# Optimization experiments

Hardware: AMD Instinct MI355X
Metric: run time of the kernel (lower is better)

The kernel has to match this reference:

```python
import jax, jax.numpy as jnp
import numpy as np

B, V, C, H, W, D = 1, 3, 32, 320, 320, 32


def setup_inputs() -> dict:
    key = jax.random.key(0)
    ks = jax.random.split(key, 14)
    feats = jax.random.normal(ks[0], (B, V, C, H, W), jnp.float32)
    # Valid pinhole projections: P = [[K @ [R|t]], [0,0,0,1]], identity rotation,
    # horizontal baselines sized so the warp stays mostly in-image over the depth range.
    K = np.array([[400.0, 0.0, W / 2.0], [0.0, 400.0, H / 2.0], [0.0, 0.0, 1.0]])
    mats = []
    for tx in (0.0, 100.0, -100.0):
        Rt = np.eye(4)
        Rt[0, 3] = tx
        P = np.eye(4)
        P[:3, :4] = K @ Rt[:3, :4]
        mats.append(P)
    proj = jnp.asarray(np.broadcast_to(np.stack(mats)[None], (B, V, 4, 4)).copy(), jnp.float32)
    planes = jnp.linspace(425.0, 935.0, D, dtype=jnp.float32)
    depth_values = jnp.broadcast_to(planes[None, :, None, None], (B, D, H, W)).astype(jnp.float32)
    s = 0.05  # small init so exp(reg_cost) stays well-scaled
    W0 = s * jax.random.normal(ks[1], (8, C, 3, 3), jnp.float32)
    Ws1 = s * jax.random.normal(ks[2], (8, 8, 3, 3), jnp.float32)
    W1 = s * jax.random.normal(ks[3], (16, 8, 3, 3), jnp.float32)
    Ws2 = s * jax.random.normal(ks[4], (16, 16, 3, 3), jnp.float32)
    W2 = s * jax.random.normal(ks[5], (32, 16, 3, 3), jnp.float32)
    Ws3 = s * jax.random.normal(ks[6], (32, 32, 3, 3), jnp.float32)
    W3 = s * jax.random.normal(ks[7], (64, 32, 3, 3), jnp.float32)
    Ws4 = s * jax.random.normal(ks[8], (64, 64, 3, 3), jnp.float32)
    U4 = s * jax.random.normal(ks[9], (32, 64, 1, 1), jnp.float32)
    U3 = s * jax.random.normal(ks[10], (16, 32, 1, 1), jnp.float32)
    U2 = s * jax.random.normal(ks[11], (8, 16, 1, 1), jnp.float32)
    Wout = s * jax.random.normal(ks[12], (1, 8, 3, 3), jnp.float32)
    return dict(feats=feats, proj=proj, depth_values=depth_values, W0=W0, Ws1=Ws1,
                W1=W1, Ws2=Ws2, W2=W2, Ws3=Ws3, W3=W3, Ws4=Ws4, U4=U4, U3=U3, U2=U2, Wout=Wout)


def _conv(x, w, stride=1):
    return jax.lax.conv_general_dilated(x, w, (stride, stride), 'SAME',
                                        dimension_numbers=('NCHW', 'OIHW', 'NCHW'))


def _up2(x):
    return jnp.repeat(jnp.repeat(x, 2, axis=2), 2, axis=3)


def _bilinear(img, x, y):
    # img [C,H,W]; x,y [N] pixel coords; zero padding, align_corners semantics
    Cc, Hh, Ww = img.shape
    x0 = jnp.floor(x)
    y0 = jnp.floor(y)
    wx = x - x0
    wy = y - y0

    def tap(xi, yi):
        valid = ((xi >= 0) & (xi <= Ww - 1) & (yi >= 0) & (yi <= Hh - 1)).astype(img.dtype)
        xc = jnp.clip(xi, 0, Ww - 1).astype(jnp.int32)
        yc = jnp.clip(yi, 0, Hh - 1).astype(jnp.int32)
        return img[:, yc, xc] * valid  # [C,N]

    return (tap(x0, y0) * (1 - wx) * (1 - wy) + tap(x0 + 1, y0) * wx * (1 - wy)
            + tap(x0, y0 + 1) * (1 - wx) * wy + tap(x0 + 1, y0 + 1) * wx * wy)


def _forward(feats, proj, depth_values, W0, Ws1, W1, Ws2, W2, Ws3, W3, Ws4, U4, U3, U2, Wout):
    Bn, Vn, Cn, Hn, Wn = feats.shape
    Dn = depth_values.shape[1]
    N = Hn * Wn
    relu = jax.nn.relu
    ref = feats[:, 0]
    ref_sq = ref * ref
    # Precompute per-src-view rotated pixel rays and translations.
    inv_ref = jnp.linalg.inv(proj[:, 0])                       # [B,4,4]
    rel = jnp.einsum('bvij,bjk->bvik', proj[:, 1:], inv_ref)   # [B,V-1,4,4]
    rot, trans = rel[:, :, :3, :3], rel[:, :, :3, 3]
    ys, xs = jnp.meshgrid(jnp.arange(Hn), jnp.arange(Wn), indexing='ij')
    pix = jnp.stack([xs.ravel(), ys.ravel(), jnp.ones(N)], 0).astype(feats.dtype)  # [3,N]
    rot_pix = jnp.einsum('bvij,jn->bvin', rot, pix)            # [B,V-1,3,N]

    def regularize(x, s1, s2, s3, s4):
        c1 = relu(_conv(x, W0) + _conv(s1, Ws1))
        c2 = relu(_conv(c1, W1, 2) + _conv(s2, Ws2))
        c3 = relu(_conv(c2, W2, 2) + _conv(s3, Ws3))
        c4 = relu(_conv(c3, W3, 2) + _conv(s4, Ws4))
        u3 = c3 + _up2(_conv(c4, U4))
        u2 = c2 + _up2(_conv(u3, U3))
        u1 = c1 + _up2(_conv(u2, U2))
        return _conv(u1, Wout), c1, c2, c3, c4

    def step(carry, depth_slice):  # depth_slice [B,H,W]
        s1, s2, s3, s4, exp_sum, depth_img, max_prob = carry
        vol_sum, vol_sq = ref, ref_sq
        dflat = depth_slice.reshape(Bn, 1, N)
        for v in range(Vn - 1):
            xyz = rot_pix[:, v] * dflat + trans[:, v, :, None]   # [B,3,N]
            px = xyz[:, 0] / xyz[:, 2]
            py = xyz[:, 1] / xyz[:, 2]
            warped = jax.vmap(_bilinear)(feats[:, v + 1], px, py).reshape(Bn, Cn, Hn, Wn)
            vol_sum = vol_sum + warped
            vol_sq = vol_sq + warped * warped
        variance = vol_sq / Vn - (vol_sum / Vn) ** 2
        cost, s1, s2, s3, s4 = regularize(variance, s1, s2, s3, s4)
        prob = jnp.exp(cost)                                     # [B,1,H,W]
        max_prob = jnp.maximum(max_prob, prob)                   # == flag*prob + (1-flag)*max
        depth_img = depth_img + depth_slice[:, None] * prob
        exp_sum = exp_sum + prob
        return (s1, s2, s3, s4, exp_sum, depth_img, max_prob), None

    z = lambda c, h, w: jnp.zeros((Bn, c, h, w), feats.dtype)
    init = (z(8, Hn, Wn), z(16, Hn // 2, Wn // 2), z(32, Hn // 4, Wn // 4), z(64, Hn // 8, Wn // 8),
            z(1, Hn, Wn), z(1, Hn, Wn), z(1, Hn, Wn))
    carry, _ = jax.lax.scan(step, init, jnp.moveaxis(depth_values, 1, 0))
    _, _, _, _, exp_sum, depth_img, max_prob = carry
    es = exp_sum + 1e-10
    depth_map = (depth_img / es)[:, 0]
    prob_map = (max_prob / es)[:, 0]
    return jnp.stack([depth_map, prob_map], axis=1)  # [B,2,H,W]


def reference(feats, proj, depth_values, W0, Ws1, W1, Ws2, W2, Ws3, W3, Ws4, U4, U3, U2, Wout):
    return _forward(feats, proj, depth_values, W0, Ws1, W1, Ws2, W2, Ws3, W3, Ws4, U4, U3, U2, Wout)
```

## Files before the change

kernel.cpp:

```cpp
#include <hip/hip_runtime.h>
#include <hip/hip_fp16.h>
#include <math.h>

#define HH 320
#define WW 320
#define NP (HH*WW)
#define CC 32
#define DD 32

#define H2 160
#define W2 160
#define N2 (H2*W2)
#define H4 80
#define W4 80
#define N4 (H4*W4)
#define H8 40
#define W8 40
#define N8 (H8*W8)

#define HALO 18
#define NHALO (HALO*HALO)

#define C1SZ (8*NP)
#define C2SZ (16*N2)
#define C3SZ (32*N4)
#define C4SZ (64*N8)

#define SMEM_FLOATS 5344

#define OFF_REL   0
#define OFF_C1R   64
#define OFF_C2R   (OFF_C1R + 5*C1SZ)
#define OFF_C3R   (OFF_C2R + 4*C2SZ)
#define OFF_C4R   (OFF_C3R + 3*C3SZ)
#define OFF_ESUM  (OFF_C4R + 2*C4SZ)
#define OFF_DIMG  (OFF_ESUM + NP)
#define OFF_MAXP  (OFF_DIMG + NP)
#define OFF_ACCE  (OFF_MAXP + NP)
#define OFF_FT    OFF_ACCE
#define OFF_END   (OFF_FT + (3*CC*NP)/2)

__global__ void k_prep(const float* __restrict__ proj, float* __restrict__ rel) {
    if (threadIdx.x != 0 || blockIdx.x != 0) return;
    float a[4][4], inv[4][4];
#pragma unroll
    for (int i = 0; i < 4; i++)
#pragma unroll
        for (int j = 0; j < 4; j++) {
            a[i][j] = proj[i*4 + j];
            inv[i][j] = (i == j) ? 1.0f : 0.0f;
        }
#pragma unroll
    for (int c = 0; c < 4; c++) {
        float s = 1.0f / a[c][c];
#pragma unroll
        for (int j = 0; j < 4; j++) { a[c][j] *= s; inv[c][j] *= s; }
#pragma unroll
        for (int r = 0; r < 4; r++) if (r != c) {
            float f = a[r][c];
#pragma unroll
            for (int j = 0; j < 4; j++) {
                a[r][j] -= f * a[c][j];
                inv[r][j] -= f * inv[c][j];
            }
        }
    }
#pragma unroll
    for (int v = 1; v < 3; v++) {
        const float* P = proj + v*16;
        float rm[3][4];
#pragma unroll
        for (int i = 0; i < 3; i++)
#pragma unroll
            for (int j = 0; j < 4; j++) {
                float s = 0.0f;
#pragma unroll
                for (int k = 0; k < 4; k++) s += P[i*4 + k] * inv[k][j];
                rm[i][j] = s;
            }
        float* o = rel + (v-1)*12;
        o[0]=rm[0][0]; o[1]=rm[0][1]; o[2]=rm[0][2];
        o[3]=rm[1][0]; o[4]=rm[1][1]; o[5]=rm[1][2];
        o[6]=rm[2][0]; o[7]=rm[2][1]; o[8]=rm[2][2];
        o[9]=rm[0][3]; o[10]=rm[1][3]; o[11]=rm[2][3];
    }
}

__global__ __launch_bounds__(256) void k_transpose(const float* __restrict__ feats,
                                                   __half* __restrict__ featsT) {
    __shared__ float lds[32][65];
    int g = blockIdx.x;
    int v = g / 1600;
    int p0 = (g - v*1600) * 64;
    const float* src = feats + (size_t)v*CC*NP + p0;
    for (int i = threadIdx.x; i < 32*64; i += 256) {
        int c = i >> 6, pp = i & 63;
        lds[c][pp] = src[(size_t)c*NP + pp];
    }
    __syncthreads();
    __half* dst = featsT + ((size_t)v*NP + p0)*32;
    int pp = threadIdx.x >> 2, cq = (threadIdx.x & 3) * 8;
    __half2 h[4];
#pragma unroll
    for (int j = 0; j < 4; j++)
        h[j] = __floats2half2_rn(lds[cq+2*j][pp], lds[cq+2*j+1][pp]);
    *(float4*)(dst + (size_t)pp*32 + cq) = *(float4*)h;
}

__device__ __forceinline__ void set_hline8(const __half* base, float* s) {
    float4 raw = *(const float4*)base;
    const __half2* h2 = (const __half2*)&raw;
#pragma unroll
    for (int j = 0; j < 4; j++) {
        float2 f = __half22float2(h2[j]);
        s[2*j]     = f.x;
        s[2*j + 1] = f.y;
    }
}
__device__ __forceinline__ void acc_hline8(const __half* base, float w, float* t) {
    float4 raw = *(const float4*)base;
    const __half2* h2 = (const __half2*)&raw;
#pragma unroll
    for (int j = 0; j < 4; j++) {
        float2 f = __half22float2(h2[j]);
        t[2*j]     += f.x * w;
        t[2*j + 1] += f.y * w;
    }
}

__device__ __forceinline__ int band_tile(int blk) { return (blk & 7) * 50 + (blk >> 3); }


__device__ void stageA(int blk, int d, int useT,
        const float* __restrict__ feats, const __half* __restrict__ featsT,
        const float* __restrict__ rel,
        const float* __restrict__ depthv, const float* __restrict__ c1r,
        const float* __restrict__ W0, const float* __restrict__ Ws1,
        float* smem) {
    __half2* pbuf = (__half2*)smem;
    float* fbuf = smem;
    const float* dslice = depthv + (size_t)d * NP;
    const float* s1 = c1r + (size_t)((d+4)%5) * C1SZ;
    float* c1out = (float*)c1r + (size_t)(d%5) * C1SZ;

    int L = band_tile(blk);
    int bx = L % 20, by = L / 20;
    int ox0 = bx*16, oy0 = by*16;

    const float inv3 = 1.0f / 3.0f;

    int opx = threadIdx.x & 15, opy = threadIdx.x >> 4;
    int obase = opy*HALO + opx;
    int outp = (oy0 + opy)*WW + ox0 + opx;

#pragma unroll 1
    for (int s = 0; s < 2; s++) {
        int hp = threadIdx.x + s*256;
        if (hp >= NHALO) break;
        int hy = hp / HALO, hx = hp - hy*HALO;
        int gy = oy0 + hy - 1, gx = ox0 + hx - 1;
        if (gy < 0 || gy >= HH || gx < 0 || gx >= WW) {
            __half2 z = __floats2half2_rn(0.0f, 0.0f);
#pragma unroll 1
            for (int c = 0; c < 16; c++) pbuf[c*NHALO + hp] = z;
            continue;
        }
        int p = gy*WW + gx;
        float depth = dslice[p];
        float fx = (float)gx, fy = (float)gy;

#pragma unroll 1
        for (int q = 0; q < 4; q++) {
            int cb = q * 8;
            float sum[8], sq[8];
            if (useT) {
                set_hline8(featsT + ((size_t)p << 5) + cb, sum);
#pragma unroll
                for (int c = 0; c < 8; c++) sq[c] = sum[c]*sum[c];
#pragma unroll
                for (int v = 0; v < 2; v++) {
                    const float* r = rel + v*12;
                    float X = (r[0]*fx + r[1]*fy + r[2]) * depth + r[9];
                    float Y = (r[3]*fx + r[4]*fy + r[5]) * depth + r[10];
                    float Z = (r[6]*fx + r[7]*fy + r[8]) * depth + r[11];
                    float iz = 1.0f / Z;
                    float px = X * iz, py = Y * iz;
                    float x0f = floorf(px), y0f = floorf(py);
                    float wx = px - x0f, wy = py - y0f;
                    int x0 = (int)x0f, y0 = (int)y0f;
                    const __half* fv = featsT + (size_t)(v+1)*CC*NP;
                    float t[8];
#pragma unroll
                    for (int c = 0; c < 8; c++) t[c] = 0.0f;
#pragma unroll
                    for (int tp = 0; tp < 4; tp++) {
                        int xi = x0 + (tp & 1), yi = y0 + (tp >> 1);
                        float wgt = ((tp & 1) ? wx : 1.0f - wx)
                                  * ((tp >> 1) ? wy : 1.0f - wy);
                        bool valid = (xi >= 0) && (xi <= WW-1) &&
                                     (yi >= 0) && (yi <= HH-1);
                        int xc = min(max(xi, 0), WW-1);
                        int yc = min(max(yi, 0), HH-1);
                        acc_hline8(fv + ((size_t)(yc*WW + xc) << 5) + cb,
                                   valid ? wgt : 0.0f, t);
                    }
#pragma unroll
                    for (int c = 0; c < 8; c++) { sum[c] += t[c]; sq[c] += t[c]*t[c]; }
                }
            } else {
#pragma unroll
                for (int c = 0; c < 8; c++) {
                    float rv = feats[(cb+c)*NP + p];
                    sum[c] = rv; sq[c] = rv*rv;
                }
#pragma unroll
                for (int v = 0; v < 2; v++) {
                    const float* r = rel + v*12;
                    float X = (r[0]*fx + r[1]*fy + r[2]) * depth + r[9];
                    float Y = (r[3]*fx + r[4]*fy + r[5]) * depth + r[10];
                    float Z = (r[6]*fx + r[7]*fy + r[8]) * depth + r[11];
                    float iz = 1.0f / Z;
                    float px = X * iz, py = Y * iz;
                    float x0f = floorf(px), y0f = floorf(py);
                    float wx = px - x0f, wy = py - y0f;
                    int x0 = (int)x0f, y0 = (int)y0f;
                    bool vax = (x0 >= 0) && (x0 < WW), vbx = (x0 >= -1) && (x0 < WW-1);
                    bool vay = (y0 >= 0) && (y0 < HH), vby = (y0 >= -1) && (y0 < HH-1);
                    int xa = min(max(x0, 0), WW-1), xb = min(max(x0+1, 0), WW-1);
                    int ya = min(max(y0, 0), HH-1), yb = min(max(y0+1, 0), HH-1);
                    int o0 = ya*WW + xa, o1 = ya*WW + xb;
                    int o2 = yb*WW + xa, o3 = yb*WW + xb;
                    float w0 = (vax && vay) ? (1.0f-wx)*(1.0f-wy) : 0.0f;
                    float w1 = (vbx && vay) ? wx*(1.0f-wy) : 0.0f;
                    float w2 = (vax && vby) ? (1.0f-wx)*wy : 0.0f;
                    float w3 = (vbx && vby) ? wx*wy : 0.0f;
                    const float* fb = feats + (size_t)(v+1)*CC*NP;
#pragma unroll 1
                    for (int c = 0; c < 8; c++) {
                        const float* b = fb + (cb+c)*NP;
                        float tv = b[o0]*w0 + b[o1]*w1 + b[o2]*w2 + b[o3]*w3;
                        sum[c] += tv; sq[c] += tv*tv;
                    }
                }
            }
#pragma unroll
            for (int c = 0; c < 4; c++) {
                float m0 = sum[2*c] * inv3,   v0 = sq[2*c] * inv3 - m0*m0;
                float m1 = sum[2*c+1] * inv3, v1 = sq[2*c+1] * inv3 - m1*m1;
                pbuf[(q*4 + c)*NHALO + hp] = __floats2half2_rn(v0, v1);
            }
        }
    }
    __syncthreads();

    float acc[8];
#pragma unroll
    for (int o = 0; o < 8; o++) acc[o] = 0.0f;

#pragma unroll 1
    for (int cp = 0; cp < 16; cp++) {
        float t0[9], t1[9];
#pragma unroll
        for (int ky = 0; ky < 3; ky++)
#pragma unroll
            for (int kx = 0; kx < 3; kx++) {
                __half2 h = pbuf[cp*NHALO + obase + ky*HALO + kx];
                t0[ky*3+kx] = __low2float(h);
                t1[ky*3+kx] = __high2float(h);
            }
#pragma unroll
        for (int o = 0; o < 8; o++) {
            const float* w0 = W0 + (o*32 + 2*cp)*9;
            float a = acc[o];
#pragma unroll
            for (int k = 0; k < 9; k++) a += t0[k] * w0[k];
#pragma unroll
            for (int k = 0; k < 9; k++) a += t1[k] * w0[9 + k];
            acc[o] = a;
        }
    }
    __syncthreads();

#pragma unroll 1
    for (int hp = threadIdx.x; hp < NHALO; hp += 256) {
        int hy = hp / HALO, hx = hp - hy*HALO;
        int gy = oy0 + hy - 1, gx = ox0 + hx - 1;
        bool v = (gy >= 0) && (gy < HH) && (gx >= 0) && (gx < WW);
        int p = v ? gy*WW + gx : 0;
#pragma unroll
        for (int c = 0; c < 8; c++) fbuf[c*NHALO + hp] = v ? s1[c*NP + p] : 0.0f;
    }
    __syncthreads();
#pragma unroll 1
    for (int ci = 0; ci < 8; ci++) {
        float t[9];
#pragma unroll
        for (int ky = 0; ky < 3; ky++)
#pragma unroll
            for (int kx = 0; kx < 3; kx++) t[ky*3+kx] = fbuf[ci*NHALO + obase + ky*HALO + kx];
#pragma unroll
        for (int o = 0; o < 8; o++) {
            const float* w = Ws1 + (o*8 + ci)*9;
            float a = acc[o];
#pragma unroll
            for (int k = 0; k < 9; k++) a += t[k] * w[k];
            acc[o] = a;
        }
    }
#pragma unroll
    for (int o = 0; o < 8; o++) c1out[o*NP + outp] = fmaxf(acc[o], 0.0f);
}

__device__ void stageB(int blk, int d,
        const float* __restrict__ c1r, const float* __restrict__ c2r_,
        const float* __restrict__ W1, const float* __restrict__ Ws2) {
    const float* c1 = c1r + (size_t)(d%5) * C1SZ;
    const float* s2 = c2r_ + (size_t)((d+3)%4) * C2SZ;
    float* c2 = (float*)c2r_ + (size_t)(d%4) * C2SZ;
    int p = (blk % 100)*256 + threadIdx.x;
    int og = blk / 100;
    int y = p / W2, x = p - y*W2;
    int offsA[9]; float mskA[9];
#pragma unroll
    for (int k = 0; k < 9; k++) {
        int yy = 2*y + k/3, xx = 2*x + k%3;
        bool v = (yy < HH) && (xx < WW);
        offsA[k] = v ? yy*WW + xx : 0;
        mskA[k] = v ? 1.0f : 0.0f;
    }
    int offsB[9]; float mskB[9];
#pragma unroll
    for (int k = 0; k < 9; k++) {
        int yy = y + k/3 - 1, xx = x + k%3 - 1;
        bool v = (yy >= 0) && (yy < H2) && (xx >= 0) && (xx < W2);
        offsB[k] = v ? yy*W2 + xx : 0;
        mskB[k] = v ? 1.0f : 0.0f;
    }
    float acc[8];
#pragma unroll
    for (int o = 0; o < 8; o++) acc[o] = 0.0f;
#pragma unroll 1
    for (int ci = 0; ci < 8; ci++) {
        const float* b = c1 + ci*NP;
        float t[9];
#pragma unroll
        for (int k = 0; k < 9; k++) t[k] = b[offsA[k]] * mskA[k];
#pragma unroll
        for (int o = 0; o < 8; o++) {
            const float* w = W1 + ((og*8 + o)*8 + ci)*9;
            float a = acc[o];
#pragma unroll
            for (int k = 0; k < 9; k++) a += t[k] * w[k];
            acc[o] = a;
        }
    }
#pragma unroll 1
    for (int ci = 0; ci < 16; ci++) {
        const float* b = s2 + ci*N2;
        float t[9];
#pragma unroll
        for (int k = 0; k < 9; k++) t[k] = b[offsB[k]] * mskB[k];
#pragma unroll
        for (int o = 0; o < 8; o++) {
            const float* w = Ws2 + ((og*8 + o)*16 + ci)*9;
            float a = acc[o];
#pragma unroll
            for (int k = 0; k < 9; k++) a += t[k] * w[k];
            acc[o] = a;
        }
    }
#pragma unroll
    for (int o = 0; o < 8; o++) c2[(og*8 + o)*N2 + p] = fmaxf(acc[o], 0.0f);
}

__device__ void stageC(int blk, int d,
        const float* __restrict__ c2r_, const float* __restrict__ c3r_,
        const float* __restrict__ W2w, const float* __restrict__ Ws3) {
    const float* c2 = c2r_ + (size_t)(d%4) * C2SZ;
    const float* s3 = c3r_ + (size_t)((d+2)%3) * C3SZ;
    float* c3 = (float*)c3r_ + (size_t)(d%3) * C3SZ;
    int p = (blk % 25)*256 + threadIdx.x;
    int og = blk / 25;
    int y = p / W4, x = p - y*W4;
    int offsA[9]; float mskA[9];
#pragma unroll
    for (int k = 0; k < 9; k++) {
        int yy = 2*y + k/3, xx = 2*x + k%3;
        bool v = (yy < H2) && (xx < W2);
        offsA[k] = v ? yy*W2 + xx : 0;
        mskA[k] = v ? 1.0f : 0.0f;
    }
    int offsB[9]; float mskB[9];
#pragma unroll
    for (int k = 0; k < 9; k++) {
        int yy = y + k/3 - 1, xx = x + k%3 - 1;
        bool v = (yy >= 0) && (yy < H4) && (xx >= 0) && (xx < W4);
        offsB[k] = v ? yy*W4 + xx : 0;
        mskB[k] = v ? 1.0f : 0.0f;
    }
    float acc[8];
#pragma unroll
    for (int o = 0; o < 8; o++) acc[o] = 0.0f;
#pragma unroll 1
    for (int ci = 0; ci < 16; ci++) {
        const float* b = c2 + ci*N2;
        float t[9];
#pragma unroll
        for (int k = 0; k < 9; k++) t[k] = b[offsA[k]] * mskA[k];
#pragma unroll
        for (int o = 0; o < 8; o++) {
            const float* w = W2w + ((og*8 + o)*16 + ci)*9;
            float a = acc[o];
#pragma unroll
            for (int k = 0; k < 9; k++) a += t[k] * w[k];
            acc[o] = a;
        }
    }
#pragma unroll 1
    for (int ci = 0; ci < 32; ci++) {
        const float* b = s3 + ci*N4;
        float t[9];
#pragma unroll
        for (int k = 0; k < 9; k++) t[k] = b[offsB[k]] * mskB[k];
#pragma unroll
        for (int o = 0; o < 8; o++) {
            const float* w = Ws3 + ((og*8 + o)*32 + ci)*9;
            float a = acc[o];
#pragma unroll
            for (int k = 0; k < 9; k++) a += t[k] * w[k];
            acc[o] = a;
        }
    }
#pragma unroll
    for (int o = 0; o < 8; o++) c3[(og*8 + o)*N4 + p] = fmaxf(acc[o], 0.0f);
}

__device__ void stageD(int blk, int d,
        const float* __restrict__ c3r_, const float* __restrict__ c4r_,
        const float* __restrict__ W3w, const float* __restrict__ Ws4) {
    const float* c3 = c3r_ + (size_t)(d%3) * C3SZ;
    const float* s4 = c4r_ + (size_t)((d+1)%2) * C4SZ;
    float* c4 = (float*)c4r_ + (size_t)(d%2) * C4SZ;
    int p = (blk % 7)*256 + threadIdx.x;
    if (p >= N8) return;
    int og = blk / 7;
    int y = p / W8, x = p - y*W8;
    int offsA[9]; float mskA[9];
#pragma unroll
    for (int k = 0; k < 9; k++) {
        int yy = 2*y + k/3, xx = 2*x + k%3;
        bool v = (yy < H4) && (xx < W4);
        offsA[k] = v ? yy*W4 + xx : 0;
        mskA[k] = v ? 1.0f : 0.0f;
    }
    int offsB[9]; float mskB[9];
#pragma unroll
    for (int k = 0; k < 9; k++) {
        int yy = y + k/3 - 1, xx = x + k%3 - 1;
        bool v = (yy >= 0) && (yy < H8) && (xx >= 0) && (xx < W8);
        offsB[k] = v ? yy*W8 + xx : 0;
        mskB[k] = v ? 1.0f : 0.0f;
    }
    float acc[8];
#pragma unroll
    for (int o = 0; o < 8; o++) acc[o] = 0.0f;
#pragma unroll 1
    for (int ci = 0; ci < 32; ci++) {
        const float* b = c3 + ci*N4;
        float t[9];
#pragma unroll
        for (int k = 0; k < 9; k++) t[k] = b[offsA[k]] * mskA[k];
#pragma unroll
        for (int o = 0; o < 8; o++) {
            const float* w = W3w + ((og*8 + o)*32 + ci)*9;
            float a = acc[o];
#pragma unroll
            for (int k = 0; k < 9; k++) a += t[k] * w[k];
            acc[o] = a;
        }
    }
#pragma unroll 1
    for (int ci = 0; ci < 64; ci++) {
        const float* b = s4 + ci*N8;
        float t[9];
#pragma unroll
        for (int k = 0; k < 9; k++) t[k] = b[offsB[k]] * mskB[k];
#pragma unroll
        for (int o = 0; o < 8; o++) {
            const float* w = Ws4 + ((og*8 + o)*64 + ci)*9;
            float a = acc[o];
#pragma unroll
            for (int k = 0; k < 9; k++) a += t[k] * w[k];
            acc[o] = a;
        }
    }
#pragma unroll
    for (int o = 0; o < 8; o++) c4[(og*8 + o)*N8 + p] = fmaxf(acc[o], 0.0f);
}

__device__ void stageU(int blk, int d,
        const float* __restrict__ c1r, const float* __restrict__ c2r_,
        const float* __restrict__ c3r_, const float* __restrict__ c4r_,
        const float* __restrict__ U4, const float* __restrict__ U3,
        const float* __restrict__ U2, const float* __restrict__ Wout,
        const float* __restrict__ depthv,
        float* __restrict__ exp_sum, float* __restrict__ depth_img,
        float* __restrict__ max_prob, float* smem) {
    const float* c1 = c1r + (size_t)(d%5) * C1SZ;
    const float* c2 = c2r_ + (size_t)(d%4) * C2SZ;
    const float* c3 = c3r_ + (size_t)(d%3) * C3SZ;
    const float* c4 = c4r_ + (size_t)(d%2) * C4SZ;
    const float* dslice = depthv + (size_t)d * NP;
    float* u3s = smem;
    float* u2s = smem + 32*36;
    float* u1s = smem + 32*36 + 16*100;

    int L = band_tile(blk);
    int bx = L % 20, by = L / 20;
    int ox0 = bx*16, oy0 = by*16;
    int qy0 = (oy0 >> 2) - 1, qx0 = (ox0 >> 2) - 1;
    int hy0 = (oy0 >> 1) - 1, hx0 = (ox0 >> 1) - 1;

#pragma unroll 1
    for (int i = threadIdx.x; i < 32*36; i += 256) {
        int ch = i / 36, pp = i - ch*36;
        int y4 = qy0 + pp/6, x4 = qx0 + pp%6;
        int y4c = min(max(y4, 0), H4-1), x4c = min(max(x4, 0), W4-1);
        int pl = (y4c >> 1)*W8 + (x4c >> 1);
        const float* w = U4 + ch*64;
        float s = c3[ch*N4 + y4c*W4 + x4c];
#pragma unroll 8
        for (int ci = 0; ci < 64; ci++) s += c4[ci*N8 + pl] * w[ci];
        u3s[ch*36 + pp] = s;
    }
    __syncthreads();
#pragma unroll 1
    for (int i = threadIdx.x; i < 16*100; i += 256) {
        int ch = i / 100, pp = i - ch*100;
        int y2 = hy0 + pp/10, x2 = hx0 + pp%10;
        int y2c = min(max(y2, 0), H2-1), x2c = min(max(x2, 0), W2-1);
        int ly = (y2c >> 1) - qy0, lx = (x2c >> 1) - qx0;
        const float* w = U3 + ch*32;
        float s = c2[ch*N2 + y2c*W2 + x2c];
#pragma unroll 8
        for (int ci = 0; ci < 32; ci++) s += u3s[ci*36 + ly*6 + lx] * w[ci];
        u2s[ch*100 + pp] = s;
    }
    __syncthreads();
#pragma unroll 1
    for (int i = threadIdx.x; i < 8*NHALO; i += 256) {
        int ch = i / NHALO, pp = i - ch*NHALO;
        int gy = oy0 + pp/HALO - 1, gx = ox0 + pp%HALO - 1;
        float s = 0.0f;
        if (gy >= 0 && gy < HH && gx >= 0 && gx < WW) {
            int ly = (gy >> 1) - hy0, lx = (gx >> 1) - hx0;
            const float* w = U2 + ch*16;
            s = c1[ch*NP + gy*WW + gx];
#pragma unroll
            for (int ci = 0; ci < 16; ci++) s += u2s[ci*100 + ly*10 + lx] * w[ci];
        }
        u1s[ch*NHALO + pp] = s;
    }
    __syncthreads();
    int px = threadIdx.x & 15, py = threadIdx.x >> 4;
    int base = py*HALO + px;
    float cost = 0.0f;
#pragma unroll 1
    for (int ci = 0; ci < 8; ci++) {
        const float* w = Wout + ci*9;
#pragma unroll
        for (int ky = 0; ky < 3; ky++)
#pragma unroll
            for (int kx = 0; kx < 3; kx++)
                cost += u1s[ci*NHALO + base + ky*HALO + kx] * w[ky*3 + kx];
    }
    int p = (oy0 + py)*WW + ox0 + px;
    float prob = expf(cost);
    exp_sum[p] += prob;
    depth_img[p] += dslice[p] * prob;
    max_prob[p] = fmaxf(max_prob[p], prob);
}

__global__ __launch_bounds__(256, 6) void k_uber(
        int t, int useT,
        const float* __restrict__ feats, const __half* __restrict__ featsT,
        const float* __restrict__ rel,
        const float* __restrict__ depthv,
        const float* __restrict__ W0, const float* __restrict__ Ws1,
        const float* __restrict__ W1, const float* __restrict__ Ws2,
        const float* __restrict__ W2w, const float* __restrict__ Ws3,
        const float* __restrict__ W3w, const float* __restrict__ Ws4,
        const float* __restrict__ U4, const float* __restrict__ U3,
        const float* __restrict__ U2, const float* __restrict__ Wout,
        float* __restrict__ c1r, float* __restrict__ c2r,
        float* __restrict__ c3r, float* __restrict__ c4r,
        float* __restrict__ esum, float* __restrict__ dimg,
        float* __restrict__ maxp) {
    __shared__ float smem[SMEM_FLOATS];
    int b = blockIdx.x;
    if (b < 400) {
        int d = t;
        if (d < DD) stageA(b, d, useT, feats, featsT, rel, depthv, c1r, W0, Ws1, smem);
    } else if (b < 600) {
        int d = t - 1;
        if (d >= 0 && d < DD) stageB(b - 400, d, c1r, c2r, W1, Ws2);
    } else if (b < 700) {
        int d = t - 2;
        if (d >= 0 && d < DD) stageC(b - 600, d, c2r, c3r, W2w, Ws3);
    } else if (b < 756) {
        int d = t - 3;
        if (d >= 0 && d < DD) stageD(b - 700, d, c3r, c4r, W3w, Ws4);
    } else {
        int d = t - 4;
        if (d >= 0 && d < DD)
            stageU(b - 756, d, c1r, c2r, c3r, c4r, U4, U3, U2, Wout, depthv,
                   esum, dimg, maxp, smem);
    }
}

__global__ __launch_bounds__(256) void k_final(
        const float* __restrict__ exp_sum, const float* __restrict__ depth_img,
        const float* __restrict__ max_prob, float* __restrict__ out) {
    int p = blockIdx.x*256 + threadIdx.x;
    if (p >= NP) return;
    float es = exp_sum[p] + 1e-10f;
    out[p] = depth_img[p] / es;
    out[NP + p] = max_prob[p] / es;
}

extern "C" void kernel_launch(void* const* d_in, const int* in_sizes, int n_in,
                              void* d_out, int out_size, void* d_ws, size_t ws_size,
                              hipStream_t stream) {
    const float* feats = (const float*)d_in[0];
    const float* proj  = (const float*)d_in[1];
    const float* depthv= (const float*)d_in[2];
    const float* W0  = (const float*)d_in[3];
    const float* Ws1 = (const float*)d_in[4];
    const float* W1  = (const float*)d_in[5];
    const float* Ws2 = (const float*)d_in[6];
    const float* W2w = (const float*)d_in[7];
    const float* Ws3 = (const float*)d_in[8];
    const float* W3w = (const float*)d_in[9];
    const float* Ws4 = (const float*)d_in[10];
    const float* U4  = (const float*)d_in[11];
    const float* U3  = (const float*)d_in[12];
    const float* U2  = (const float*)d_in[13];
    const float* Wout= (const float*)d_in[14];

    float* ws = (float*)d_ws;
    float* rel  = ws + OFF_REL;
    float* c1r  = ws + OFF_C1R;
    float* c2r  = ws + OFF_C2R;
    float* c3r  = ws + OFF_C3R;
    float* c4r  = ws + OFF_C4R;
    float* esum = ws + OFF_ESUM;
    float* dimg = ws + OFF_DIMG;
    float* maxp = ws + OFF_MAXP;

    int useT = (ws_size >= (size_t)OFF_END * sizeof(float)) ? 1 : 0;
    __half* featsT = (__half*)(useT ? (ws + OFF_FT) : ws);

    hipMemsetAsync(c1r, 0, (size_t)(OFF_ACCE - OFF_C1R) * sizeof(float), stream);
    k_prep<<<1, 1, 0, stream>>>(proj, rel);
    if (useT)
        k_transpose<<<dim3(3*1600), 256, 0, stream>>>(feats, featsT);

    for (int t = 0; t < DD + 4; t++) {
        k_uber<<<dim3(1156), 256, 0, stream>>>(t, useT, feats, featsT, rel, depthv,
            W0, Ws1, W1, Ws2, W2w, Ws3, W3w, Ws4, U4, U3, U2, Wout,
            c1r, c2r, c3r, c4r, esum, dimg, maxp);
    }
    k_final<<<dim3(400), 256, 0, stream>>>(esum, dimg, maxp, (float*)d_out);
}
```

Baseline: 2.577 ms.

## Split stage A into 16x8 tiles with output channels divided across thread halves

Stage A now handles 16x8 output tiles instead of 16x16, so it launches twice as many blocks (800). Each thread computes one halo pixel's variance features with no second loop pass. In the convolution phase, two groups of 128 threads each produce 4 of the 8 output channels. The goal is more parallelism and less per-thread serial work in the heaviest stage, at the cost of more halo recomputation (180 halo pixels per 128 outputs versus 324 per 256) and a larger grid.

```diff
diff --git a/kernel.cpp b/kernel.cpp
--- a/kernel.cpp
+++ b/kernel.cpp
@@ -17,6 +17,10 @@
 #define H8 40
 #define W8 40
 #define N8 (H8*W8)
+
+#define HAW 18
+#define HAH 10
+#define NHA (HAW*HAH)
 
 #define HALO 18
 #define NHALO (HALO*HALO)
@@ -128,7 +132,8 @@
     }
 }
 
-__device__ __forceinline__ int band_tile(int blk) { return (blk & 7) * 50 + (blk >> 3); }
+__device__ __forceinline__ int band_tileU(int blk) { return (blk & 7) * 50  + (blk >> 3); }
+__device__ __forceinline__ int band_tileA(int blk) { return (blk & 7) * 100 + (blk >> 3); }
 
 
 __device__ void stageA(int blk, int d, int useT,
@@ -143,119 +148,117 @@
     const float* s1 = c1r + (size_t)((d+4)%5) * C1SZ;
     float* c1out = (float*)c1r + (size_t)(d%5) * C1SZ;
 
-    int L = band_tile(blk);
+    int L = band_tileA(blk);
     int bx = L % 20, by = L / 20;
-    int ox0 = bx*16, oy0 = by*16;
+    int ox0 = bx*16, oy0 = by*8;
 
     const float inv3 = 1.0f / 3.0f;
 
-    int opx = threadIdx.x & 15, opy = threadIdx.x >> 4;
-    int obase = opy*HALO + opx;
-    int outp = (oy0 + opy)*WW + ox0 + opx;
-
-#pragma unroll 1
-    for (int s = 0; s < 2; s++) {
-        int hp = threadIdx.x + s*256;
-        if (hp >= NHALO) break;
-        int hy = hp / HALO, hx = hp - hy*HALO;
+    int hp = threadIdx.x;
+    if (hp < NHA) {
+        int hy = hp / HAW, hx = hp - hy*HAW;
         int gy = oy0 + hy - 1, gx = ox0 + hx - 1;
         if (gy < 0 || gy >= HH || gx < 0 || gx >= WW) {
             __half2 z = __floats2half2_rn(0.0f, 0.0f);
 #pragma unroll 1
-            for (int c = 0; c < 16; c++) pbuf[c*NHALO + hp] = z;
-            continue;
-        }
-        int p = gy*WW + gx;
-        float depth = dslice[p];
-        float fx = (float)gx, fy = (float)gy;
-
-#pragma unroll 1
-        for (int q = 0; q < 4; q++) {
-            int cb = q * 8;
-            float sum[8], sq[8];
-            if (useT) {
-                set_hline8(featsT + ((size_t)p << 5) + cb, sum);
-#pragma unroll
-                for (int c = 0; c < 8; c++) sq[c] = sum[c]*sum[c];
-#pragma unroll
-                for (int v = 0; v < 2; v++) {
-                    const float* r = rel + v*12;
-                    float X = (r[0]*fx + r[1]*fy + r[2]) * depth + r[9];
-                    float Y = (r[3]*fx + r[4]*fy + r[5]) * depth + r[10];
-                    float Z = (r[6]*fx + r[7]*fy + r[8]) * depth + r[11];
-                    float iz = 1.0f / Z;
-                    float px = X * iz, py = Y * iz;
-                    float x0f = floorf(px), y0f = floorf(py);
-                    float wx = px - x0f, wy = py - y0f;
-                    int x0 = (int)x0f, y0 = (int)y0f;
-                    const __half* fv = featsT + (size_t)(v+1)*CC*NP;
-                    float t[8];
-#pragma unroll
-                    for (int c = 0; c < 8; c++) t[c] = 0.0f;
-#pragma unroll
-                    for (int tp = 0; tp < 4; tp++) {
-                        int xi = x0 + (tp & 1), yi = y0 + (tp >> 1);
-                        float wgt = ((tp & 1) ? wx : 1.0f - wx)
-                                  * ((tp >> 1) ? wy : 1.0f - wy);
-                        bool valid = (xi >= 0) && (xi <= WW-1) &&
-                                     (yi >= 0) && (yi <= HH-1);
-                        int xc = min(max(xi, 0), WW-1);
-                        int yc = min(max(yi, 0), HH-1);
-                        acc_hline8(fv + ((size_t)(yc*WW + xc) << 5) + cb,
-                                   valid ? wgt : 0.0f, t);
+            for (int c = 0; c < 16; c++) pbuf[c*NHA + hp] = z;
+        } else {
+            int p = gy*WW + gx;
+            float depth = dslice[p];
+            float fx = (float)gx, fy = (float)gy;
+
+#pragma unroll 1
+            for (int q = 0; q < 4; q++) {
+                int cb = q * 8;
+                float sum[8], sq[8];
+                if (useT) {
+                    set_hline8(featsT + ((size_t)p << 5) + cb, sum);
+#pragma unroll
+                    for (int c = 0; c < 8; c++) sq[c] = sum[c]*sum[c];
+#pragma unroll
+                    for (int v = 0; v < 2; v++) {
+                        const float* r = rel + v*12;
+                        float X = (r[0]*fx + r[1]*fy + r[2]) * depth + r[9];
+                        float Y = (r[3]*fx + r[4]*fy + r[5]) * depth + r[10];
+                        float Z = (r[6]*fx + r[7]*fy + r[8]) * depth + r[11];
+                        float iz = 1.0f / Z;
+                        float px = X * iz, py = Y * iz;
+                        float x0f = floorf(px), y0f = floorf(py);
+                        float wx = px - x0f, wy = py - y0f;
+                        int x0 = (int)x0f, y0 = (int)y0f;
+                        const __half* fv = featsT + (size_t)(v+1)*CC*NP;
+                        float t[8];
+#pragma unroll
+                        for (int c = 0; c < 8; c++) t[c] = 0.0f;
+#pragma unroll
+                        for (int tp = 0; tp < 4; tp++) {
+                            int xi = x0 + (tp & 1), yi = y0 + (tp >> 1);
+                            float wgt = ((tp & 1) ? wx : 1.0f - wx)
+                                      * ((tp >> 1) ? wy : 1.0f - wy);
+                            bool valid = (xi >= 0) && (xi <= WW-1) &&
+                                         (yi >= 0) && (yi <= HH-1);
+                            int xc = min(max(xi, 0), WW-1);
+                            int yc = min(max(yi, 0), HH-1);
+                            acc_hline8(fv + ((size_t)(yc*WW + xc) << 5) + cb,
+                                       valid ? wgt : 0.0f, t);
+                        }
+#pragma unroll
+                        for (int c = 0; c < 8; c++) { sum[c] += t[c]; sq[c] += t[c]*t[c]; }
                     }
-#pragma unroll
-                    for (int c = 0; c < 8; c++) { sum[c] += t[c]; sq[c] += t[c]*t[c]; }
-                }
-            } else {
-#pragma unroll
-                for (int c = 0; c < 8; c++) {
-                    float rv = feats[(cb+c)*NP + p];
-                    sum[c] = rv; sq[c] = rv*rv;
-                }
-#pragma unroll
-                for (int v = 0; v < 2; v++) {
-                    const float* r = rel + v*12;
-                    float X = (r[0]*fx + r[1]*fy + r[2]) * depth + r[9];
-                    float Y = (r[3]*fx + r[4]*fy + r[5]) * depth + r[10];
-                    float Z = (r[6]*fx + r[7]*fy + r[8]) * depth + r[11];
-                    float iz = 1.0f / Z;
-                    float px = X * iz, py = Y * iz;
-                    float x0f = floorf(px), y0f = floorf(py);
-                    float wx = px - x0f, wy = py - y0f;
-                    int x0 = (int)x0f, y0 = (int)y0f;
-                    bool vax = (x0 >= 0) && (x0 < WW), vbx = (x0 >= -1) && (x0 < WW-1);
-                    bool vay = (y0 >= 0) && (y0 < HH), vby = (y0 >= -1) && (y0 < HH-1);
-                    int xa = min(max(x0, 0), WW-1), xb = min(max(x0+1, 0), WW-1);
-                    int ya = min(max(y0, 0), HH-1), yb = min(max(y0+1, 0), HH-1);
-                    int o0 = ya*WW + xa, o1 = ya*WW + xb;
-                    int o2 = yb*WW + xa, o3 = yb*WW + xb;
-                    float w0 = (vax && vay) ? (1.0f-wx)*(1.0f-wy) : 0.0f;
-                    float w1 = (vbx && vay) ? wx*(1.0f-wy) : 0.0f;
-                    float w2 = (vax && vby) ? (1.0f-wx)*wy : 0.0f;
-                    float w3 = (vbx && vby) ? wx*wy : 0.0f;
-                    const float* fb = feats + (size_t)(v+1)*CC*NP;
-#pragma unroll 1
+                } else {
+#pragma unroll
                     for (int c = 0; c < 8; c++) {
-                        const float* b = fb + (cb+c)*NP;
-                        float tv = b[o0]*w0 + b[o1]*w1 + b[o2]*w2 + b[o3]*w3;
-                        sum[c] += tv; sq[c] += tv*tv;
+                        float rv = feats[(cb+c)*NP + p];
+                        sum[c] = rv; sq[c] = rv*rv;
+                    }
+#pragma unroll
+                    for (int v = 0; v < 2; v++) {
+                        const float* r = rel + v*12;
+                        float X = (r[0]*fx + r[1]*fy + r[2]) * depth + r[9];
+                        float Y = (r[3]*fx + r[4]*fy + r[5]) * depth + r[10];
+                        float Z = (r[6]*fx + r[7]*fy + r[8]) * depth + r[11];
+                        float iz = 1.0f / Z;
+                        float px = X * iz, py = Y * iz;
+                        float x0f = floorf(px), y0f = floorf(py);
+                        float wx = px - x0f, wy = py - y0f;
+                        int x0 = (int)x0f, y0 = (int)y0f;
+                        bool vax = (x0 >= 0) && (x0 < WW), vbx = (x0 >= -1) && (x0 < WW-1);
+                        bool vay = (y0 >= 0) && (y0 < HH), vby = (y0 >= -1) && (y0 < HH-1);
+                        int xa = min(max(x0, 0), WW-1), xb = min(max(x0+1, 0), WW-1);
+                        int ya = min(max(y0, 0), HH-1), yb = min(max(y0+1, 0), HH-1);
+                        int o0 = ya*WW + xa, o1 = ya*WW + xb;
+                        int o2 = yb*WW + xa, o3 = yb*WW + xb;
+                        float w0 = (vax && vay) ? (1.0f-wx)*(1.0f-wy) : 0.0f;
+                        float w1 = (vbx && vay) ? wx*(1.0f-wy) : 0.0f;
+                        float w2 = (vax && vby) ? (1.0f-wx)*wy : 0.0f;
+                        float w3 = (vbx && vby) ? wx*wy : 0.0f;
+                        const float* fb = feats + (size_t)(v+1)*CC*NP;
+#pragma unroll 1
+                        for (int c = 0; c < 8; c++) {
+                            const float* b = fb + (cb+c)*NP;
+                            float tv = b[o0]*w0 + b[o1]*w1 + b[o2]*w2 + b[o3]*w3;
+                            sum[c] += tv; sq[c] += tv*tv;
+                        }
                     }
                 }
+#pragma unroll
+                for (int c = 0; c < 4; c++) {
+                    float m0 = sum[2*c] * inv3,   v0 = sq[2*c] * inv3 - m0*m0;
+                    float m1 = sum[2*c+1] * inv3, v1 = sq[2*c+1] * inv3 - m1*m1;
+                    pbuf[(q*4 + c)*NHA + hp] = __floats2half2_rn(v0, v1);
+                }
             }
-#pragma unroll
-            for (int c = 0; c < 4; c++) {
-                float m0 = sum[2*c] * inv3,   v0 = sq[2*c] * inv3 - m0*m0;
-                float m1 = sum[2*c+1] * inv3, v1 = sq[2*c+1] * inv3 - m1*m1;
-                pbuf[(q*4 + c)*NHALO + hp] = __floats2half2_rn(v0, v1);
-            }
         }
     }
     __syncthreads();
 
-    float acc[8];
-#pragma unroll
-    for (int o = 0; o < 8; o++) acc[o] = 0.0f;
+    int px_ = threadIdx.x & 127;
+    int og  = threadIdx.x >> 7;
+    int opy = px_ >> 4, opx = px_ & 15;
+    int obase = opy*HAW + opx;
+    float acc[4];
+#pragma unroll
+    for (int o = 0; o < 4; o++) acc[o] = 0.0f;
 
 #pragma unroll 1
     for (int cp = 0; cp < 16; cp++) {
@@ -264,13 +267,13 @@
         for (int ky = 0; ky < 3; ky++)
 #pragma unroll
             for (int kx = 0; kx < 3; kx++) {
-                __half2 h = pbuf[cp*NHALO + obase + ky*HALO + kx];
+                __half2 h = pbuf[cp*NHA + obase + ky*HAW + kx];
                 t0[ky*3+kx] = __low2float(h);
                 t1[ky*3+kx] = __high2float(h);
             }
 #pragma unroll
-        for (int o = 0; o < 8; o++) {
-            const float* w0 = W0 + (o*32 + 2*cp)*9;
+        for (int o = 0; o < 4; o++) {
+            const float* w0 = W0 + ((og*4 + o)*32 + 2*cp)*9;
             float a = acc[o];
 #pragma unroll
             for (int k = 0; k < 9; k++) a += t0[k] * w0[k];
@@ -281,14 +284,13 @@
     }
     __syncthreads();
 
-#pragma unroll 1
-    for (int hp = threadIdx.x; hp < NHALO; hp += 256) {
-        int hy = hp / HALO, hx = hp - hy*HALO;
+    if (hp < NHA) {
+        int hy = hp / HAW, hx = hp - hy*HAW;
         int gy = oy0 + hy - 1, gx = ox0 + hx - 1;
         bool v = (gy >= 0) && (gy < HH) && (gx >= 0) && (gx < WW);
         int p = v ? gy*WW + gx : 0;
 #pragma unroll
-        for (int c = 0; c < 8; c++) fbuf[c*NHALO + hp] = v ? s1[c*NP + p] : 0.0f;
+        for (int c = 0; c < 8; c++) fbuf[c*NHA + hp] = v ? s1[c*NP + p] : 0.0f;
     }
     __syncthreads();
 #pragma unroll 1
@@ -297,18 +299,19 @@
 #pragma unroll
         for (int ky = 0; ky < 3; ky++)
 #pragma unroll
-            for (int kx = 0; kx < 3; kx++) t[ky*3+kx] = fbuf[ci*NHALO + obase + ky*HALO + kx];
-#pragma unroll
-        for (int o = 0; o < 8; o++) {
-            const float* w = Ws1 + (o*8 + ci)*9;
+            for (int kx = 0; kx < 3; kx++) t[ky*3+kx] = fbuf[ci*NHA + obase + ky*HAW + kx];
+#pragma unroll
+        for (int o = 0; o < 4; o++) {
+            const float* w = Ws1 + ((og*4 + o)*8 + ci)*9;
             float a = acc[o];
 #pragma unroll
             for (int k = 0; k < 9; k++) a += t[k] * w[k];
             acc[o] = a;
         }
     }
-#pragma unroll
-    for (int o = 0; o < 8; o++) c1out[o*NP + outp] = fmaxf(acc[o], 0.0f);
+    int outp = (oy0 + opy)*WW + ox0 + opx;
+#pragma unroll
+    for (int o = 0; o < 4; o++) c1out[(og*4 + o)*NP + outp] = fmaxf(acc[o], 0.0f);
 }
 
 __device__ void stageB(int blk, int d,
@@ -515,7 +518,7 @@
     float* u2s = smem + 32*36;
     float* u1s = smem + 32*36 + 16*100;
 
-    int L = band_tile(blk);
+    int L = band_tileU(blk);
     int bx = L % 20, by = L / 20;
     int ox0 = bx*16, oy0 = by*16;
     int qy0 = (oy0 >> 2) - 1, qx0 = (ox0 >> 2) - 1;
@@ -598,22 +601,22 @@
         float* __restrict__ maxp) {
     __shared__ float smem[SMEM_FLOATS];
     int b = blockIdx.x;
-    if (b < 400) {
+    if (b < 800) {
         int d = t;
         if (d < DD) stageA(b, d, useT, feats, featsT, rel, depthv, c1r, W0, Ws1, smem);
-    } else if (b < 600) {
+    } else if (b < 1000) {
         int d = t - 1;
-        if (d >= 0 && d < DD) stageB(b - 400, d, c1r, c2r, W1, Ws2);
-    } else if (b < 700) {
+        if (d >= 0 && d < DD) stageB(b - 800, d, c1r, c2r, W1, Ws2);
+    } else if (b < 1100) {
         int d = t - 2;
-        if (d >= 0 && d < DD) stageC(b - 600, d, c2r, c3r, W2w, Ws3);
-    } else if (b < 756) {
+        if (d >= 0 && d < DD) stageC(b - 1000, d, c2r, c3r, W2w, Ws3);
+    } else if (b < 1156) {
         int d = t - 3;
-        if (d >= 0 && d < DD) stageD(b - 700, d, c3r, c4r, W3w, Ws4);
+        if (d >= 0 && d < DD) stageD(b - 1100, d, c3r, c4r, W3w, Ws4);
     } else {
         int d = t - 4;
         if (d >= 0 && d < DD)
-            stageU(b - 756, d, c1r, c2r, c3r, c4r, U4, U3, U2, Wout, depthv,
+            stageU(b - 1156, d, c1r, c2r, c3r, c4r, U4, U3, U2, Wout, depthv,
                    esum, dimg, maxp, smem);
     }
 }
@@ -666,7 +669,7 @@
         k_transpose<<<dim3(3*1600), 256, 0, stream>>>(feats, featsT);
 
     for (int t = 0; t < DD + 4; t++) {
-        k_uber<<<dim3(1156), 256, 0, stream>>>(t, useT, feats, featsT, rel, depthv,
+        k_uber<<<dim3(1556), 256, 0, stream>>>(t, useT, feats, featsT, rel, depthv,
             W0, Ws1, W1, Ws2, W2w, Ws3, W3w, Ws4, U4, U3, U2, Wout,
             c1r, c2r, c3r, c4r, esum, dimg, maxp);
     }
```

Result: slower. 3.520 ms (+36.6%).
